# Optimization experiments

Hardware: AMD Instinct MI355X
Metric: run time of the kernel (lower is better)

The kernel has to match this reference:

```python
import jax, jax.numpy as jnp
import numpy as np

COMMITMENT_COST = 0.25


def setup_inputs() -> dict:
    key = jax.random.key(0)
    k1, k2 = jax.random.split(key)
    z = jax.random.normal(k1, (32, 256, 32, 32), dtype=jnp.float32)
    # Embedding init mirrors uniform(-1/codebook_size, 1/codebook_size)
    emb = jax.random.uniform(k2, (4096, 256), dtype=jnp.float32,
                             minval=-1.0 / 4096, maxval=1.0 / 4096)
    return {"z": z, "emb": emb}


def reference(z, emb):
    # z: [b, c, h, w] with c == token_size; emb: [codebook_size, token_size]
    b, c, h, w = z.shape
    z_bhwc = jnp.transpose(z, (0, 2, 3, 1))           # [b, h, w, c]
    z_flat = z_bhwc.reshape(-1, c)                    # [N, c]

    # Squared-distance matrix: ||z||^2 + ||e||^2 - 2 z e^T  -> [N, K]
    d = (jnp.sum(z_flat * z_flat, axis=1, keepdims=True)
         + jnp.sum(emb * emb, axis=1)
         - 2.0 * jnp.einsum('nd,kd->nk', z_flat, emb))

    idx = jnp.argmin(d, axis=1)                       # [N]
    z_q = emb[idx].reshape(z_bhwc.shape)              # [b, h, w, c]

    commitment_loss = COMMITMENT_COST * jnp.mean(
        (jax.lax.stop_gradient(z_q) - z_bhwc) ** 2)
    codebook_loss = jnp.mean((z_q - jax.lax.stop_gradient(z_bhwc)) ** 2)
    loss = commitment_loss + codebook_loss

    # Straight-through estimator
    z_q = z_bhwc + jax.lax.stop_gradient(z_q - z_bhwc)
    z_q = jnp.transpose(z_q, (0, 3, 1, 2))            # [b, c, h, w]

    min_encoding_indices = idx.reshape(b, h, w)
    return z_q, loss, commitment_loss, codebook_loss, min_encoding_indices
```

## Files before the change

kernel.cpp:

```cpp
#include <hip/hip_runtime.h>

#define CDIM 256
#define CB   4096
#define HW   1024
#define NTOK 32768
#define NELEM 8388608
#define MARGIN 3.5e-4f
#define OVCAP 64

typedef float f32x4 __attribute__((ext_vector_type(4)));
typedef short bf16x8 __attribute__((ext_vector_type(8)));
typedef unsigned int u32;
typedef unsigned long long u64;

__device__ __forceinline__ unsigned short f2bf(float x) {
    u32 b = __float_as_uint(x);
    return (unsigned short)((b + 0x7fffu + ((b >> 16) & 1u)) >> 16);
}
__device__ __forceinline__ u32 fenc(float f) {
    u32 b = __float_as_uint(f);
    return (b & 0x80000000u) ? ~b : (b | 0x80000000u);
}
__device__ __forceinline__ float fdec(u32 u) {
    return __uint_as_float((u & 0x80000000u) ? (u & 0x7fffffffu) : ~u);
}
__device__ __forceinline__ u64 shfl_xor_u64(u64 v, int s) {
    u32 lo = __shfl_xor((u32)v, s);
    u32 hi = __shfl_xor((u32)(v >> 32), s);
    return ((u64)hi << 32) | lo;
}
__device__ __forceinline__ void gl_lds16(const void* g, void* l) {
    __builtin_amdgcn_global_load_lds(
        (const __attribute__((address_space(1))) u32*)g,
        (__attribute__((address_space(3))) u32*)l, 16, 0, 0);
}


__global__ __launch_bounds__(256) void prep(const float* __restrict__ z,
                                            const float* __restrict__ emb,
                                            float* __restrict__ zT,
                                            unsigned short* __restrict__ z_hip,
                                            float* __restrict__ zn,
                                            u32* __restrict__ ovcnt,
                                            float* __restrict__ enorm2,
                                            unsigned short* __restrict__ e_hip,
                                            u32* __restrict__ cnt2) {
    __shared__ float T[32][132];
    const int tid = threadIdx.x;
    if (blockIdx.x >= 256) {
        const int cg = blockIdx.x - 256;
        const int code_l = tid >> 1;
        const int code = cg * 128 + code_l;
        const int sxz = (code_l >> 1) & 3;
        float s = 0.f;
#pragma unroll
        for (int kb = 0; kb < 4; ++kb) {
            const int c0 = (tid & 1) * 128 + kb * 32;
            const int kc = c0 >> 5;
            __align__(16) unsigned short tmp[32];
#pragma unroll
            for (int q = 0; q < 8; ++q) {
                float4 v = *(const float4*)(emb + (size_t)code * CDIM + c0 + 4 * q);
                s += v.x * v.x + v.y * v.y + v.z * v.z + v.w * v.w;
                tmp[4 * q + 0] = f2bf(v.x); tmp[4 * q + 1] = f2bf(v.y);
                tmp[4 * q + 2] = f2bf(v.z); tmp[4 * q + 3] = f2bf(v.w);
            }
            uint4* dst4 = (uint4*)(e_hip + (((size_t)(cg * 8 + kc) * 128 + code_l) * 32));
#pragma unroll
            for (int q = 0; q < 4; ++q)
                dst4[q ^ sxz] = *(uint4*)&tmp[8 * q];
        }
        s += __shfl_xor(s, 1);
        if ((tid & 1) == 0) enorm2[code] = s;
        if (cg == 0 && tid == 0) *cnt2 = 0u;
        return;
    }
    const int rg = blockIdx.x;
    const int b = (rg * 128) >> 10, hw0 = (rg * 128) & 1023;
    const float* zb = z + (size_t)b * (CDIM * HW) + hw0;
    const int tt = tid >> 1, h = (tid & 1) * 16;
    const int q0 = h >> 3;
    const int sxz = (tt >> 1) & 3;
    float zsq = 0.f;
    for (int kc = 0; kc < 8; ++kc) {
        const int c0 = kc * 32;
        __syncthreads();
#pragma unroll
        for (int p = 0; p < 16; ++p) {
            const int c = p * 2 + (tid >> 7);
            T[c][tid & 127] = zb[(size_t)(c0 + c) * HW + (tid & 127)];
        }
        __syncthreads();
        float* dstT = zT + (size_t)(rg * 128 + tt) * CDIM + c0 + h;
        __align__(16) unsigned short us[16];
#pragma unroll
        for (int q = 0; q < 4; ++q) {
            float4 v;
            v.x = T[h + 4 * q + 0][tt]; v.y = T[h + 4 * q + 1][tt];
            v.z = T[h + 4 * q + 2][tt]; v.w = T[h + 4 * q + 3][tt];
            ((float4*)dstT)[q] = v;
            zsq += v.x * v.x + v.y * v.y + v.z * v.z + v.w * v.w;
            us[4 * q + 0] = f2bf(v.x); us[4 * q + 1] = f2bf(v.y);
            us[4 * q + 2] = f2bf(v.z); us[4 * q + 3] = f2bf(v.w);
        }
        uint4* d4 = (uint4*)(z_hip + (((size_t)(rg * 8 + kc) * 128 + tt) * 32));
        d4[q0 ^ sxz]       = *(uint4*)&us[0];
        d4[(q0 + 1) ^ sxz] = *(uint4*)&us[8];
    }
    zsq += __shfl_xor(zsq, 1);
    if ((tid & 1) == 0) {
        const int t = rg * 128 + tt;
        zn[t] = zsq; ovcnt[t] = 0u;
    }
}


__global__ __launch_bounds__(256, 4) void p1(const unsigned short* __restrict__ z_hip,
                                             const unsigned short* __restrict__ e_hip,
                                             const float* __restrict__ enorm2,
                                             u64* __restrict__ cand,
                                             u32* __restrict__ ovcnt,
                                             u64* __restrict__ ovslot) {
    __shared__ __align__(16) unsigned short Bs[2][128 * 32];
    const int bid = blockIdx.x;
    const int rg = bid >> 5, cg = bid & 31;
    const int tid = threadIdx.x;
    const int w = tid >> 6, lane = tid & 63;
    const int quad = lane >> 4, l15 = lane & 15;
    const int swz = (quad ^ ((l15 >> 1) & 3)) * 8;

    f32x4 acc[2][8];
#pragma unroll
    for (int i = 0; i < 2; ++i)
#pragma unroll
        for (int j = 0; j < 8; ++j)
#pragma unroll
            for (int e = 0; e < 4; ++e) acc[i][j][e] = 0.f;

    const char* gB = (const char*)e_hip + ((size_t)cg << 16) + w * 2048 + lane * 16;
    const char* gA0 = (const char*)z_hip + ((size_t)rg << 16)
                      + (w * 32 + l15) * 64 + swz * 2;
    char* lB = (char*)Bs + w * 2048;
    gl_lds16(gB, lB);           gl_lds16(gB + 1024, lB + 1024);
    gB += 8192;
    bf16x8 af0 = *(const bf16x8*)(gA0);
    bf16x8 af1 = *(const bf16x8*)(gA0 + 1024);
    __syncthreads();
#pragma unroll
    for (int kc = 0; kc < 8; ++kc) {
        const int cur = kc & 1;
        bf16x8 afn0, afn1;
        if (kc < 7) {
            char* dB = lB + (cur ^ 1) * 8192;
            gl_lds16(gB, dB);       gl_lds16(gB + 1024, dB + 1024);
            gB += 8192;
            const char* gA = gA0 + (size_t)(kc + 1) * 8192;
            afn0 = *(const bf16x8*)(gA);
            afn1 = *(const bf16x8*)(gA + 1024);
        }
        const unsigned short* B0 = Bs[cur];
#pragma unroll
        for (int nh = 0; nh < 2; ++nh) {
            bf16x8 bfr[4];
#pragma unroll
            for (int nj = 0; nj < 4; ++nj)
                bfr[nj] = *(const bf16x8*)&B0[((nh * 4 + nj) * 16 + l15) * 32 + swz];
#pragma unroll
            for (int nj = 0; nj < 4; ++nj) {
                acc[0][nh * 4 + nj] = __builtin_amdgcn_mfma_f32_16x16x32_bf16(
                    af0, bfr[nj], acc[0][nh * 4 + nj], 0, 0, 0);
                acc[1][nh * 4 + nj] = __builtin_amdgcn_mfma_f32_16x16x32_bf16(
                    af1, bfr[nj], acc[1][nh * 4 + nj], 0, 0, 0);
            }
        }
        if (kc < 7) {
            af0 = afn0; af1 = afn1;
            __syncthreads();
        }
    }
    float en[8];
#pragma unroll
    for (int ni = 0; ni < 8; ++ni) en[ni] = enorm2[cg * 128 + ni * 16 + l15];
#pragma unroll
    for (int mi = 0; mi < 2; ++mi) {
#pragma unroll
        for (int r = 0; r < 4; ++r) {
            const int row = w * 32 + mi * 16 + quad * 4 + r;
            const int t = rg * 128 + row;
            float dv[8];
#pragma unroll
            for (int ni = 0; ni < 8; ++ni) dv[ni] = en[ni] - 2.0f * acc[mi][ni][r];
            float m = fminf(fminf(fminf(dv[0], dv[1]), fminf(dv[2], dv[3])),
                            fminf(fminf(dv[4], dv[5]), fminf(dv[6], dv[7])));
            m = fminf(m, __shfl_xor(m, 1));
            m = fminf(m, __shfl_xor(m, 2));
            m = fminf(m, __shfl_xor(m, 4));
            m = fminf(m, __shfl_xor(m, 8));
            u32 myni = 8u;
#pragma unroll
            for (int ni = 7; ni >= 0; --ni)
                if (dv[ni] == m) myni = (u32)ni;
            const unsigned long long bal = __ballot(myni < 8u);
            const int sl = __ffs((u32)((bal >> (quad << 4)) & 0xFFFFu)) - 1;
            if (l15 == sl) {
                const u32 k = (u32)(cg * 128 + (int)myni * 16 + l15);
                cand[((size_t)t << 5) + cg] = ((u64)fenc(m) << 32) | k;
            }
            const float thr = m + MARGIN;
#pragma unroll
            for (int ni = 0; ni < 8; ++ni) {
                if (dv[ni] <= thr && !(l15 == sl && ni == (int)myni)) {
                    const u32 k = (u32)(cg * 128 + ni * 16 + l15);
                    const u32 pos = atomicAdd(&ovcnt[t], 1u);
                    if (pos < (u32)OVCAP)
                        ovslot[(size_t)t * OVCAP + pos] = ((u64)fenc(dv[ni]) << 32) | k;
                }
            }
        }
    }
}

__global__ __launch_bounds__(256) void k5(const float* __restrict__ zT,
                                          const float* __restrict__ emb,
                                          const float* __restrict__ enorm2,
                                          const float* __restrict__ zn,
                                          const u64* __restrict__ cand,
                                          const u32* __restrict__ ovcnt,
                                          const u64* __restrict__ ovslot,
                                          float* __restrict__ idxf,
                                          float* __restrict__ dmin) {
    const int t = (blockIdx.x * 256 + threadIdx.x) >> 6;
    const int lane = threadIdx.x & 63;
    const u64 pkv = cand[((size_t)t << 5) + (lane & 31)];
    u64 g = pkv;
#pragma unroll
    for (int s = 1; s < 32; s <<= 1) {
        const u64 o = shfl_xor_u64(g, s);
        g = o < g ? o : g;
    }
    const float thr = fdec((u32)(g >> 32)) + MARGIN;
    const float4 za = ((const float4*)(zT + (size_t)t * CDIM))[lane];
    const float znv = zn[t];
    float bdv = 1e30f; int bk = 0x7fffffff;
    unsigned long long q = __ballot(fdec((u32)(pkv >> 32)) <= thr)
                           & 0xFFFFFFFFull;
    while (q) {
        const int i = __ffsll(q) - 1; q &= q - 1;
        const int k = __shfl((int)(u32)pkv, i);
        const float4 ea = ((const float4*)(emb + (size_t)k * CDIM))[lane];
        float p = za.x * ea.x + za.y * ea.y + za.z * ea.z + za.w * ea.w;
#pragma unroll
        for (int s = 1; s < 64; s <<= 1) p += __shfl_xor(p, s);
        const float t1 = znv + enorm2[k];
        const float d = t1 - 2.0f * p;
        if (d < bdv || (d == bdv && k < bk)) { bdv = d; bk = k; }
    }
    u32 n = ovcnt[t]; if (n > (u32)OVCAP) n = (u32)OVCAP;
    for (u32 i = 0; i < n; ++i) {
        const u64 ov = ovslot[(size_t)t * OVCAP + i];
        if (!(fdec((u32)(ov >> 32)) <= thr)) continue;
        const int k = (int)(u32)ov;
        const float4 ea = ((const float4*)(emb + (size_t)k * CDIM))[lane];
        float p = za.x * ea.x + za.y * ea.y + za.z * ea.z + za.w * ea.w;
#pragma unroll
        for (int s = 1; s < 64; s <<= 1) p += __shfl_xor(p, s);
        const float t1 = znv + enorm2[k];
        const float d = t1 - 2.0f * p;
        if (d < bdv || (d == bdv && k < bk)) { bdv = d; bk = k; }
    }
    if (lane == 0) {
        idxf[t] = (float)bk;
        dmin[t] = bdv;
    }
}

__global__ __launch_bounds__(256) void k2(const float* __restrict__ emb,
                                          const float* __restrict__ idxf,
                                          const float* __restrict__ dmin,
                                          float* __restrict__ zq,
                                          float* __restrict__ out3,
                                          u32* __restrict__ cnt2) {
    __shared__ int ks[64];
    __shared__ float red[256];
    __shared__ int lastFlag;
    const int tid = threadIdx.x;
    const int tok0 = blockIdx.x * 64;
    const int b = tok0 >> 10, hw0 = tok0 & 1023;
    if (tid < 64) ks[tid] = (int)idxf[tok0 + tid];
    __syncthreads();
    const int t4 = (tid & 15) * 4;
    const int ka = ks[t4], kb = ks[t4 + 1], kc = ks[t4 + 2], kd = ks[t4 + 3];
    float* outb = zq + (size_t)b * (CDIM * HW) + hw0 + t4;
    int c = tid >> 4;
#pragma unroll
    for (int p = 0; p < 16; ++p, c += 16) {
        float4 v;
        v.x = emb[(size_t)ka * CDIM + c];
        v.y = emb[(size_t)kb * CDIM + c];
        v.z = emb[(size_t)kc * CDIM + c];
        v.w = emb[(size_t)kd * CDIM + c];
        *(float4*)(outb + (size_t)c * HW) = v;
    }
    if (tid == 0) lastFlag = (atomicAdd(cnt2, 1u) == 511u) ? 1 : 0;
    __syncthreads();
    if (lastFlag) {
        const float4* d4 = (const float4*)dmin;
        float s = 0.f;
        for (int i = tid; i < NTOK / 4; i += 256) {
            const float4 v = d4[i];
            s += (v.x + v.y) + (v.z + v.w);
        }
        red[tid] = s;
        __syncthreads();
        for (int o = 128; o > 0; o >>= 1) {
            if (tid < o) red[tid] += red[tid + o];
            __syncthreads();
        }
        if (tid == 0) {
            const float mse = red[0] / (float)NELEM;
            out3[0] = 1.25f * mse;
            out3[1] = 0.25f * mse;
            out3[2] = mse;
        }
    }
}

extern "C" void kernel_launch(void* const* d_in, const int* in_sizes, int n_in,
                              void* d_out, int out_size, void* d_ws, size_t ws_size,
                              hipStream_t stream) {
    const float* z   = (const float*)d_in[0];
    const float* emb = (const float*)d_in[1];
    float* out = (float*)d_out;
    char* w = (char*)d_ws;

    float* zn     = (float*)w;                       w += NTOK * 4;
    float* enorm2 = (float*)w;                       w += CB * 4;
    u32*   ovcnt  = (u32*)w;                         w += NTOK * 4;
    float* dmin   = (float*)w;                       w += NTOK * 4;
    u32*   cnt2   = (u32*)w;                         w += 256;
    float* zT     = (float*)w;                       w += (size_t)NTOK * CDIM * 4;
    unsigned short* z_hip = (unsigned short*)w;      w += (size_t)NTOK * CDIM * 2;
    unsigned short* e_hip = (unsigned short*)w;      w += (size_t)CB * CDIM * 2;
    u64*   cand   = (u64*)w;                         w += (size_t)NTOK * 32 * 8;
    u64*   ovslot = (u64*)w;                         w += (size_t)NTOK * OVCAP * 8;
    float* idxf = out + NELEM + 3;

    hipLaunchKernelGGL(prep, dim3(256 + 32),  dim3(256), 0, stream,
                       z, emb, zT, z_hip, zn, ovcnt, enorm2, e_hip, cnt2);
    hipLaunchKernelGGL(p1,  dim3((NTOK / 128) * (CB / 128)), dim3(256), 0, stream,
                       z_hip, e_hip, enorm2, cand, ovcnt, ovslot);
    hipLaunchKernelGGL(k5,  dim3(NTOK / 4),   dim3(256), 0, stream,
                       zT, emb, enorm2, zn, cand, ovcnt, ovslot, idxf, dmin);
    hipLaunchKernelGGL(k2,  dim3(NTOK / 64),  dim3(256), 0, stream,
                       emb, idxf, dmin, out, out + NELEM, cnt2);
}
```

Baseline: 273.5 us.

## Double per-block token tile in p1 GEMM and relax barrier waits

Each p1 block now covers 256 tokens instead of 128 (each wave handles 64 rows with 4 A fragments), so every LDS-staged codebook tile is reused across twice as many tokens and the grid is halved. A fragments are double-buffered in registers, and the full __syncthreads is replaced by a partial vmcnt wait plus a raw s_barrier so the A prefetch loads can remain in flight. Launch bounds drop from 4 to 2 blocks per CU to make room for 128 accumulator floats per thread. This risks lower occupancy and makes correctness depend on hand-counted outstanding global loads.

Measured after the change: 323.7 us. +18.4%, slower.

```diff
diff --git a/kernel.cpp b/kernel.cpp
--- a/kernel.cpp
+++ b/kernel.cpp
@@ -115,7 +115,7 @@
 }
 
 
-__global__ __launch_bounds__(256, 4) void p1(const unsigned short* __restrict__ z_hip,
+__global__ __launch_bounds__(256, 2) void p1(const unsigned short* __restrict__ z_hip,
                                              const unsigned short* __restrict__ e_hip,
                                              const float* __restrict__ enorm2,
                                              u64* __restrict__ cand,
@@ -129,34 +129,39 @@
     const int quad = lane >> 4, l15 = lane & 15;
     const int swz = (quad ^ ((l15 >> 1) & 3)) * 8;
 
-    f32x4 acc[2][8];
-#pragma unroll
-    for (int i = 0; i < 2; ++i)
+    f32x4 acc[4][8];
+#pragma unroll
+    for (int i = 0; i < 4; ++i)
 #pragma unroll
         for (int j = 0; j < 8; ++j)
 #pragma unroll
             for (int e = 0; e < 4; ++e) acc[i][j][e] = 0.f;
 
     const char* gB = (const char*)e_hip + ((size_t)cg << 16) + w * 2048 + lane * 16;
-    const char* gA0 = (const char*)z_hip + ((size_t)rg << 16)
-                      + (w * 32 + l15) * 64 + swz * 2;
+    const int gz = 2 * rg + (w >> 1);
+    const int rl0 = (w & 1) * 64;
+    const char* gA0 = (const char*)z_hip + ((size_t)gz << 16)
+                      + (rl0 + l15) * 64 + swz * 2;
     char* lB = (char*)Bs + w * 2048;
     gl_lds16(gB, lB);           gl_lds16(gB + 1024, lB + 1024);
     gB += 8192;
-    bf16x8 af0 = *(const bf16x8*)(gA0);
-    bf16x8 af1 = *(const bf16x8*)(gA0 + 1024);
+    bf16x8 afr[2][4];
+#pragma unroll
+    for (int mi = 0; mi < 4; ++mi)
+        afr[0][mi] = *(const bf16x8*)(gA0 + mi * 1024);
     __syncthreads();
 #pragma unroll
     for (int kc = 0; kc < 8; ++kc) {
         const int cur = kc & 1;
-        bf16x8 afn0, afn1;
         if (kc < 7) {
             char* dB = lB + (cur ^ 1) * 8192;
             gl_lds16(gB, dB);       gl_lds16(gB + 1024, dB + 1024);
             gB += 8192;
+            asm volatile("" ::: "memory");
             const char* gA = gA0 + (size_t)(kc + 1) * 8192;
-            afn0 = *(const bf16x8*)(gA);
-            afn1 = *(const bf16x8*)(gA + 1024);
+#pragma unroll
+            for (int mi = 0; mi < 4; ++mi)
+                afr[cur ^ 1][mi] = *(const bf16x8*)(gA + mi * 1024);
         }
         const unsigned short* B0 = Bs[cur];
 #pragma unroll
@@ -166,27 +171,27 @@
             for (int nj = 0; nj < 4; ++nj)
                 bfr[nj] = *(const bf16x8*)&B0[((nh * 4 + nj) * 16 + l15) * 32 + swz];
 #pragma unroll
-            for (int nj = 0; nj < 4; ++nj) {
-                acc[0][nh * 4 + nj] = __builtin_amdgcn_mfma_f32_16x16x32_bf16(
-                    af0, bfr[nj], acc[0][nh * 4 + nj], 0, 0, 0);
-                acc[1][nh * 4 + nj] = __builtin_amdgcn_mfma_f32_16x16x32_bf16(
-                    af1, bfr[nj], acc[1][nh * 4 + nj], 0, 0, 0);
-            }
+            for (int mi = 0; mi < 4; ++mi)
+#pragma unroll
+                for (int nj = 0; nj < 4; ++nj)
+                    acc[mi][nh * 4 + nj] = __builtin_amdgcn_mfma_f32_16x16x32_bf16(
+                        afr[cur][mi], bfr[nj], acc[mi][nh * 4 + nj], 0, 0, 0);
         }
         if (kc < 7) {
-            af0 = afn0; af1 = afn1;
-            __syncthreads();
+            asm volatile("s_waitcnt vmcnt(4)" ::: "memory");
+            __builtin_amdgcn_s_barrier();
+            asm volatile("" ::: "memory");
         }
     }
     float en[8];
 #pragma unroll
     for (int ni = 0; ni < 8; ++ni) en[ni] = enorm2[cg * 128 + ni * 16 + l15];
 #pragma unroll
-    for (int mi = 0; mi < 2; ++mi) {
+    for (int mi = 0; mi < 4; ++mi) {
 #pragma unroll
         for (int r = 0; r < 4; ++r) {
-            const int row = w * 32 + mi * 16 + quad * 4 + r;
-            const int t = rg * 128 + row;
+            const int row_local = rl0 + mi * 16 + quad * 4 + r;
+            const int t = gz * 128 + row_local;
             float dv[8];
 #pragma unroll
             for (int ni = 0; ni < 8; ++ni) dv[ni] = en[ni] - 2.0f * acc[mi][ni][r];
@@ -347,7 +352,7 @@
 
     hipLaunchKernelGGL(prep, dim3(256 + 32),  dim3(256), 0, stream,
                        z, emb, zT, z_hip, zn, ovcnt, enorm2, e_hip, cnt2);
-    hipLaunchKernelGGL(p1,  dim3((NTOK / 128) * (CB / 128)), dim3(256), 0, stream,
+    hipLaunchKernelGGL(p1,  dim3((NTOK / 256) * (CB / 128)), dim3(256), 0, stream,
                        z_hip, e_hip, enorm2, cand, ovcnt, ovslot);
     hipLaunchKernelGGL(k5,  dim3(NTOK / 4),   dim3(256), 0, stream,
                        zT, emb, enorm2, zn, cand, ovcnt, ovslot, idxf, dmin);
```
